# Performance work log

Hardware: AMD Instinct MI355X
Metric: run time of the kernel (lower is better)

## Reference

```python
import jax, jax.numpy as jnp
import numpy as np

B, N, F_IN, T = 8, 1024, 32, 24
E = 16384
K = 3
C_CHEB = 64
C_TIME = 64
TIME_STRIDES = 1
LN_EPS = 1e-5


def setup_inputs() -> dict:
    key = jax.random.key(0)
    ks = jax.random.split(key, 20)
    s = 0.05
    return dict(
        X=jax.random.normal(ks[0], (B, N, F_IN, T), jnp.float32),
        edge_index=jax.random.randint(ks[1], (2, E), 0, N, dtype=jnp.int32),
        # TemporalAttention params
        U1=jax.random.uniform(ks[2], (N,), jnp.float32),
        U2=jax.random.normal(ks[3], (F_IN, N), jnp.float32) * s,
        U3=jax.random.uniform(ks[4], (F_IN,), jnp.float32),
        be=jax.random.normal(ks[5], (1, T, T), jnp.float32) * s,
        Ve=jax.random.normal(ks[6], (T, T), jnp.float32) * s,
        # SpatialAttention params
        W1=jax.random.uniform(ks[7], (T,), jnp.float32),
        W2=jax.random.normal(ks[8], (F_IN, T), jnp.float32) * s,
        W3=jax.random.uniform(ks[9], (F_IN,), jnp.float32),
        bs=jax.random.normal(ks[10], (1, N, N), jnp.float32) * s,
        Vs=jax.random.normal(ks[11], (N, N), jnp.float32) * s,
        # ChebConvAttention params
        cheb_W=jax.random.normal(ks[12], (K, F_IN, C_CHEB), jnp.float32) * s,
        cheb_b=jax.random.uniform(ks[13], (C_CHEB,), jnp.float32),
        # time conv (1x3) and residual conv (1x1), OIHW
        time_W=jax.random.normal(ks[14], (C_TIME, C_CHEB, 1, 3), jnp.float32) * s,
        time_b=jax.random.uniform(ks[15], (C_TIME,), jnp.float32),
        res_W=jax.random.normal(ks[16], (C_TIME, F_IN, 1, 1), jnp.float32) * s,
        res_b=jax.random.uniform(ks[17], (C_TIME,), jnp.float32),
        # layer norm over nb_time_filter channels
        ln_g=jax.random.uniform(ks[18], (C_TIME,), jnp.float32),
        ln_b=jax.random.uniform(ks[19], (C_TIME,), jnp.float32),
    )


def _astgcn_block(X, edge_index, U1, U2, U3, be, Ve, W1, W2, W3, bs, Vs,
                  cheb_W, cheb_b, time_W, time_b, res_W, res_b, ln_g, ln_b):
    Bn, Nn, Fn, Tn = X.shape
    # ---- temporal attention: E_att [B,T,T] ----
    lhs = jnp.einsum('bnft,n->btf', X, U1) @ U2               # [B,T,N]
    rhs = jnp.einsum('f,bnft->bnt', U3, X)                    # [B,N,T]
    Escore = jnp.einsum('ij,bjk->bik', Ve,
                        jax.nn.sigmoid(jnp.einsum('btn,bnu->btu', lhs, rhs) + be))
    E_att = jax.nn.softmax(Escore, axis=1)
    Xt = (X.reshape(Bn, Nn * Fn, Tn) @ E_att).reshape(Bn, Nn, Fn, Tn)
    # ---- spatial attention: S [B,N,N] ----
    slhs = jnp.einsum('bnft,t->bnf', Xt, W1) @ W2             # [B,N,T]
    srhs = jnp.einsum('f,bnft->btn', W3, Xt)                  # [B,T,N]
    Sscore = jnp.einsum('ij,bjk->bik', Vs, jax.nn.sigmoid(slhs @ srhs + bs))
    S = jax.nn.softmax(Sscore, axis=1)
    # ---- scaled Laplacian edge norm (sym normalization, lambda_max = 2) ----
    row, col = edge_index[0], edge_index[1]
    w = (row != col).astype(X.dtype)                          # remove self loops
    deg = jax.ops.segment_sum(w, row, num_segments=Nn)
    dis = jnp.where(deg > 0, jax.lax.rsqrt(jnp.where(deg > 0, deg, 1.0)), 0.0)
    norm = -dis[row] * w * dis[col]                           # [E]; the +1/-1 self loops cancel
    att_norm = norm[None, :] * S[:, row, col]                 # [B,E]

    def prop(x, coef):
        # out[b, r] += coef[(b,)e] * x[b, c] for each edge e=(r,c); x: [B,N,F,T]
        c = coef[None, :, None, None] if coef.ndim == 1 else coef[:, :, None, None]
        msg = c * x[:, col]                                   # [B,E,F,T]
        return jnp.zeros_like(x).at[:, row].add(msg)

    diagS = jnp.diagonal(S, axis1=1, axis2=2)                 # [B,N]
    Tx0 = diagS[:, :, None, None] * X                         # [B,N,F,T]
    out = jnp.einsum('bnft,fo->bnot', Tx0, cheb_W[0])
    Tx1 = prop(Tx0, att_norm)
    out = out + jnp.einsum('bnft,fo->bnot', Tx1, cheb_W[1])
    for k in range(2, cheb_W.shape[0]):
        Tx2 = 2.0 * prop(Tx1, norm) - Tx0
        out = out + jnp.einsum('bnft,fo->bnot', Tx2, cheb_W[k])
        Tx0, Tx1 = Tx1, Tx2
    X_hat = jax.nn.relu(out + cheb_b[None, None, :, None])    # [B,N,Ccheb,T]
    # ---- temporal conv + residual conv + layer norm ----
    dn = ('NCHW', 'OIHW', 'NCHW')
    t_out = jax.lax.conv_general_dilated(
        X_hat.transpose(0, 2, 1, 3), time_W,
        window_strides=(1, TIME_STRIDES), padding=((0, 0), (1, 1)),
        dimension_numbers=dn) + time_b[None, :, None, None]   # [B,Ctime,N,T']
    r_out = jax.lax.conv_general_dilated(
        X.transpose(0, 2, 1, 3), res_W,
        window_strides=(1, TIME_STRIDES), padding=((0, 0), (0, 0)),
        dimension_numbers=dn) + res_b[None, :, None, None]    # [B,Ctime,N,T']
    Z = jax.nn.relu(r_out + t_out).transpose(0, 3, 2, 1)      # [B,T',N,Ctime]
    mu = Z.mean(axis=-1, keepdims=True)
    var = Z.var(axis=-1, keepdims=True)
    Z = (Z - mu) * jax.lax.rsqrt(var + LN_EPS) * ln_g + ln_b
    return Z.transpose(0, 2, 3, 1)                            # [B,N,Ctime,T']


def reference(X, edge_index, U1, U2, U3, be, Ve, W1, W2, W3, bs, Vs,
              cheb_W, cheb_b, time_W, time_b, res_W, res_b, ln_g, ln_b):
    return _astgcn_block(X, edge_index, U1, U2, U3, be, Ve, W1, W2, W3, bs, Vs,
                         cheb_W, cheb_b, time_W, time_b, res_W, res_b, ln_g, ln_b)
```

## Files before the change

### kernel.cpp

```cpp
#include <hip/hip_runtime.h>
#include <hip/hip_bf16.h>
#include <math.h>

#define B_ 8
#define N_ 1024
#define F_ 32
#define T_ 24
#define E_ 16384
#define CC_ 64
#define CT_ 64
#define LN_EPS_ 1e-5f

typedef __attribute__((ext_vector_type(8))) short bf16x8;
typedef __attribute__((ext_vector_type(4))) float f32x4;

__device__ __forceinline__ short f2bf(float f) {
    union { float f; unsigned u; } v; v.f = f;
    unsigned r = v.u + 0x7fffu + ((v.u >> 16) & 1u);
    return (short)(r >> 16);
}


__global__ __launch_bounds__(768) void k_lhs2(const float* __restrict__ X,
                                              const float* __restrict__ U1,
                                              float* __restrict__ out) {
    __shared__ float su[64];
    int b = blockIdx.x >> 4;
    int n0 = (blockIdx.x & 15) * 64;
    int tid = threadIdx.x;
    if (tid < 64) su[tid] = U1[n0 + tid];
    __syncthreads();
    float acc = 0.f;
    const float* xp = X + ((size_t)b * N_ + n0) * 768 + tid;
#pragma unroll 8
    for (int i = 0; i < 64; ++i) acc += xp[(size_t)i * 768] * su[i];
    int f = tid / 24, t = tid - (tid / 24) * 24;
    atomicAdd(&out[b * 768 + t * 32 + f], acc);
}

__global__ void k_lhsN(const float* __restrict__ lhs_tf, const float* __restrict__ U2,
                       float* __restrict__ out) {
    int idx = blockIdx.x * 256 + threadIdx.x;
    if (idx >= B_ * T_ * N_) return;
    int n = idx % N_;
    int bt = idx / N_;
    float acc = 0.f;
#pragma unroll
    for (int f = 0; f < F_; ++f) acc += lhs_tf[bt * F_ + f] * U2[(size_t)f * N_ + n];
    out[idx] = acc;
}

__global__ void k_rhsT(const float* __restrict__ X, const float* __restrict__ U3,
                       float* __restrict__ out) {
    int idx = blockIdx.x * 256 + threadIdx.x;
    if (idx >= B_ * N_ * T_) return;
    int t = idx % T_;
    int n = (idx / T_) % N_;
    int b = idx / (N_ * T_);
    const float* xp = X + ((size_t)(b * N_ + n) * F_) * T_ + t;
    float acc = 0.f;
#pragma unroll
    for (int f = 0; f < F_; ++f) acc += U3[f] * xp[f * T_];
    out[idx] = acc;
}

__global__ __launch_bounds__(256) void k_transp(const float* __restrict__ in,
                                                float* __restrict__ outp) {
    __shared__ float s[64 * 25];
    int b = blockIdx.x >> 4;
    int n0 = (blockIdx.x & 15) * 64;
    int tid = threadIdx.x;
    const float* ip = in + ((size_t)b * N_ + n0) * 24;
    for (int q = tid; q < 1536; q += 256) s[(q / 24) * 25 + (q % 24)] = ip[q];
    __syncthreads();
    for (int q = tid; q < 1536; q += 256) {
        int t = q >> 6, n = q & 63;
        outp[((size_t)b * 24 + t) * N_ + n0 + n] = s[n * 25 + t];
    }
}

__global__ __launch_bounds__(64) void k_edot(const float* __restrict__ lhsN,
                                             const float* __restrict__ rhsTT,
                                             const float* __restrict__ be,
                                             float* __restrict__ sig) {
    int blk = blockIdx.x;
    int b = blk / 576, ij = blk % 576;
    int i = ij / 24, j = ij % 24;
    int lane = threadIdx.x;
    const float* lp = lhsN + ((size_t)b * 24 + i) * N_;
    const float* rp = rhsTT + ((size_t)b * 24 + j) * N_;
    float acc = 0.f;
#pragma unroll
    for (int n = lane; n < N_; n += 64) acc += lp[n] * rp[n];
    for (int off = 32; off > 0; off >>= 1) acc += __shfl_xor(acc, off);
    if (lane == 0) sig[blk] = 1.f / (1.f + expf(-(acc + be[ij])));
}

__global__ __launch_bounds__(576) void k_eatt2(const float* __restrict__ sig,
                                               const float* __restrict__ Ve,
                                               float* __restrict__ Eatt) {
    __shared__ float ss[T_ * T_];
    __shared__ float esc[T_ * T_];
    int b = blockIdx.x;
    int tid = threadIdx.x;
    ss[tid] = sig[b * 576 + tid];
    __syncthreads();
    int i = tid / T_, j = tid % T_;
    {
        float acc = 0.f;
#pragma unroll
        for (int m = 0; m < T_; ++m) acc += Ve[i * T_ + m] * ss[m * T_ + j];
        esc[tid] = acc;
    }
    __syncthreads();
    if (tid < T_) {
        int jj = tid;
        float mx = -1e30f;
        for (int r = 0; r < T_; ++r) mx = fmaxf(mx, esc[r * T_ + jj]);
        float s = 0.f;
        for (int r = 0; r < T_; ++r) {
            float e = expf(esc[r * T_ + jj] - mx);
            ss[r * T_ + jj] = e;
            s += e;
        }
        float inv = 1.f / s;
        for (int r = 0; r < T_; ++r) Eatt[(size_t)(b * T_ + r) * T_ + jj] = ss[r * T_ + jj] * inv;
    }
}

__global__ void k_xt(const float* __restrict__ X, const float* __restrict__ Eatt,
                     float* __restrict__ Xt) {
    __shared__ float e[T_ * T_];
    const int per_b = N_ * F_ * T_ / 256;
    int b = blockIdx.x / per_b;
    int tid = threadIdx.x;
    for (int q = tid; q < T_ * T_; q += 256) e[q] = Eatt[(size_t)b * T_ * T_ + q];
    __syncthreads();
    int off = (blockIdx.x % per_b) * 256 + tid;
    int t = off % T_;
    int nf = off / T_;
    const float* xr = X + ((size_t)b * N_ * F_ + nf) * T_;
    float acc = 0.f;
#pragma unroll
    for (int k = 0; k < T_; ++k) acc += xr[k] * e[k * T_ + t];
    Xt[((size_t)b * N_ * F_ + nf) * T_ + t] = acc;
}


__global__ void k_slhsF(const float* __restrict__ Xt, const float* __restrict__ W1,
                        float* __restrict__ out) {
    int idx = blockIdx.x * 256 + threadIdx.x;
    if (idx >= B_ * N_ * F_) return;
    const float* xp = Xt + (size_t)idx * T_;
    float acc = 0.f;
#pragma unroll
    for (int t = 0; t < T_; ++t) acc += xp[t] * W1[t];
    out[idx] = acc;
}

__global__ void k_slhs(const float* __restrict__ slhsF, const float* __restrict__ W2,
                       float* __restrict__ out) {
    int idx = blockIdx.x * 256 + threadIdx.x;
    if (idx >= B_ * N_ * T_) return;
    int t = idx % T_;
    int bn = idx / T_;
    float acc = 0.f;
#pragma unroll
    for (int f = 0; f < F_; ++f) acc += slhsF[(size_t)bn * F_ + f] * W2[f * T_ + t];
    out[idx] = acc;
}

__global__ void k_srhs(const float* __restrict__ Xt, const float* __restrict__ W3,
                       float* __restrict__ out) {
    int idx = blockIdx.x * 256 + threadIdx.x;
    if (idx >= B_ * N_ * T_) return;
    int t = idx % T_;
    int n = (idx / T_) % N_;
    int b = idx / (N_ * T_);
    const float* xp = Xt + ((size_t)(b * N_ + n) * F_) * T_ + t;
    float acc = 0.f;
#pragma unroll
    for (int f = 0; f < F_; ++f) acc += W3[f] * xp[f * T_];
    out[((size_t)b * T_ + t) * N_ + n] = acc;
}

__global__ __launch_bounds__(256) void k_psig2(const float* __restrict__ slhs,
                                               const float* __restrict__ srhs,
                                               const float* __restrict__ bs,
                                               float* __restrict__ Psig,
                                               __hip_bfloat16* __restrict__ PsigT) {
    __shared__ float sl[64][24];
    __shared__ float sr[24][64];
    __shared__ short st[64][72];
    int b = blockIdx.z;
    int i0 = blockIdx.y * 64, k0 = blockIdx.x * 64;
    int tid = threadIdx.x;
    {
        const float* sp = slhs + ((size_t)b * N_ + i0) * 24;
#pragma unroll
        for (int it = 0; it < 6; ++it) {
            int q = tid + it * 256;
            sl[q / 24][q % 24] = sp[q];
        }
        const float* rp = srhs + (size_t)b * 24 * N_ + k0;
#pragma unroll
        for (int it = 0; it < 6; ++it) {
            int q = tid + it * 256;
            sr[q >> 6][q & 63] = rp[(size_t)(q >> 6) * N_ + (q & 63)];
        }
    }
    __syncthreads();
    int ib = (tid >> 4) * 4;
    int kb = (tid & 15) * 4;
    float acc[4][4];
#pragma unroll
    for (int a = 0; a < 4; ++a) {
        const float4 bv = *(const float4*)(bs + (size_t)(i0 + ib + a) * N_ + k0 + kb);
        acc[a][0] = bv.x; acc[a][1] = bv.y; acc[a][2] = bv.z; acc[a][3] = bv.w;
    }
#pragma unroll
    for (int t = 0; t < 24; ++t) {
        float r0 = sr[t][kb], r1 = sr[t][kb + 1], r2 = sr[t][kb + 2], r3 = sr[t][kb + 3];
#pragma unroll
        for (int a = 0; a < 4; ++a) {
            float lv = sl[ib + a][t];
            acc[a][0] += lv * r0; acc[a][1] += lv * r1; acc[a][2] += lv * r2; acc[a][3] += lv * r3;
        }
    }
#pragma unroll
    for (int a = 0; a < 4; ++a) {
        float4 o;
        o.x = 1.f / (1.f + expf(-acc[a][0]));
        o.y = 1.f / (1.f + expf(-acc[a][1]));
        o.z = 1.f / (1.f + expf(-acc[a][2]));
        o.w = 1.f / (1.f + expf(-acc[a][3]));
        *(float4*)(Psig + (size_t)((size_t)b * N_ + i0 + ib + a) * N_ + k0 + kb) = o;
        st[kb + 0][ib + a] = f2bf(o.x);
        st[kb + 1][ib + a] = f2bf(o.y);
        st[kb + 2][ib + a] = f2bf(o.z);
        st[kb + 3][ib + a] = f2bf(o.w);
    }
    __syncthreads();
    short* op = (short*)PsigT + ((size_t)b * N_ + k0) * N_ + i0;
#pragma unroll
    for (int it = 0; it < 2; ++it) {
        int ch = tid + it * 256;
        int kk = ch >> 3, off = (ch & 7) * 8;
        uint4 u = *(uint4*)&st[kk][off];
        *(uint4*)(op + (size_t)kk * N_ + off) = u;
    }
}

__global__ __launch_bounds__(256) void k_smfma(const float* __restrict__ Vs,
                                               const __hip_bfloat16* __restrict__ PsigT,
                                               float* __restrict__ S) {
    __shared__ short Asd[128][40];
    __shared__ short Bsd[128][40];
    const int b = blockIdx.z;
    const int bm = blockIdx.y * 128, bn = blockIdx.x * 128;
    const int tid = threadIdx.x;
    const int lane = tid & 63, wave = tid >> 6;
    const int wr = wave >> 1, wc = wave & 1;
    const int fr = lane & 15, ks = lane >> 4;
    f32x4 acc[4][4] = {};
    const short* PT = (const short*)PsigT + (size_t)b * N_ * N_;
    for (int k0 = 0; k0 < N_; k0 += 32) {
#pragma unroll
        for (int it = 0; it < 4; ++it) {
            int q = tid + it * 256;
            int row = q >> 3, kk = (q & 7) * 4;
            float4 v = *(const float4*)(Vs + (size_t)(bm + row) * N_ + k0 + kk);
            short4 s4;
            s4.x = f2bf(v.x); s4.y = f2bf(v.y); s4.z = f2bf(v.z); s4.w = f2bf(v.w);
            *(short4*)&Asd[row][kk] = s4;
        }
#pragma unroll
        for (int it = 0; it < 2; ++it) {
            int q = tid + it * 256;
            int row = q >> 2, kk = (q & 3) * 8;
            uint4 u = *(const uint4*)(PT + (size_t)(bn + row) * N_ + k0 + kk);
            *(uint4*)&Bsd[row][kk] = u;
        }
        __syncthreads();
        bf16x8 a[4], bf[4];
#pragma unroll
        for (int m = 0; m < 4; ++m) a[m] = *(const bf16x8*)&Asd[wr * 64 + m * 16 + fr][ks * 8];
#pragma unroll
        for (int n = 0; n < 4; ++n) bf[n] = *(const bf16x8*)&Bsd[wc * 64 + n * 16 + fr][ks * 8];
#pragma unroll
        for (int m = 0; m < 4; ++m)
#pragma unroll
            for (int n = 0; n < 4; ++n)
                acc[m][n] = __builtin_amdgcn_mfma_f32_16x16x32_bf16(a[m], bf[n], acc[m][n], 0, 0, 0);
        __syncthreads();
    }
    float* Sb = S + (size_t)b * N_ * N_;
#pragma unroll
    for (int m = 0; m < 4; ++m)
#pragma unroll
        for (int n = 0; n < 4; ++n) {
#pragma unroll
            for (int j = 0; j < 4; ++j) {
                int row = bm + wr * 64 + m * 16 + (lane >> 4) * 4 + j;
                int col = bn + wc * 64 + n * 16 + (lane & 15);
                Sb[(size_t)row * N_ + col] = acc[m][n][j];
            }
        }
}

__global__ __launch_bounds__(256) void k_smpart(const float* __restrict__ S,
                                                float* __restrict__ pmax,
                                                float* __restrict__ psum) {
    __shared__ float tile[128][64];
    __shared__ float redm[4][64];
    __shared__ float reds[4][64];
    int b = blockIdx.z;
    int chunk = blockIdx.y;
    int cg = blockIdx.x;
    int tid = threadIdx.x;
    const float* Sb = S + (size_t)b * N_ * N_ + (size_t)(chunk * 128) * N_ + cg * 64;
    for (int q = tid; q < 8192; q += 256) {
        int r = q >> 6, c = q & 63;
        tile[r][c] = Sb[(size_t)r * N_ + c];
    }
    __syncthreads();
    int c = tid & 63, grp = tid >> 6;
    float m = -1e30f;
    for (int r = grp; r < 128; r += 4) m = fmaxf(m, tile[r][c]);
    redm[grp][c] = m;
    __syncthreads();
    m = fmaxf(fmaxf(redm[0][c], redm[1][c]), fmaxf(redm[2][c], redm[3][c]));
    float s = 0.f;
    for (int r = grp; r < 128; r += 4) s += __expf(tile[r][c] - m);
    reds[grp][c] = s;
    __syncthreads();
    if (grp == 0) {
        s = reds[0][c] + reds[1][c] + reds[2][c] + reds[3][c];
        size_t o = ((size_t)b * 8 + chunk) * N_ + cg * 64 + c;
        pmax[o] = m;
        psum[o] = s;
    }
}

__global__ __launch_bounds__(1024) void k_smcomb(const float* __restrict__ pmax,
                                                 const float* __restrict__ psum,
                                                 float* __restrict__ colMax,
                                                 float* __restrict__ colInv) {
    int b = blockIdx.x;
    int col = threadIdx.x;
    float M = -1e30f;
#pragma unroll
    for (int ch = 0; ch < 8; ++ch) M = fmaxf(M, pmax[((size_t)b * 8 + ch) * N_ + col]);
    float s = 0.f;
#pragma unroll
    for (int ch = 0; ch < 8; ++ch)
        s += psum[((size_t)b * 8 + ch) * N_ + col] *
             __expf(pmax[((size_t)b * 8 + ch) * N_ + col] - M);
    colMax[(size_t)b * N_ + col] = M;
    colInv[(size_t)b * N_ + col] = 1.f / s;
}


__global__ void k_count(const int* __restrict__ rowI, const int* __restrict__ colI,
                        int* __restrict__ cnt, float* __restrict__ deg) {
    int e = blockIdx.x * 256 + threadIdx.x;
    if (e >= E_) return;
    int r = rowI[e];
    atomicAdd(&cnt[r], 1);
    if (r != colI[e]) atomicAdd(&deg[r], 1.0f);
}

__global__ __launch_bounds__(1024) void k_scan(const int* __restrict__ cnt,
                                               const float* __restrict__ deg,
                                               int* __restrict__ rowPtr,
                                               int* __restrict__ fillPos,
                                               float* __restrict__ dis) {
    __shared__ int s[N_];
    int tid = threadIdx.x;
    int my = cnt[tid];
    s[tid] = my;
    __syncthreads();
    for (int off = 1; off < N_; off <<= 1) {
        int v = 0;
        if (tid >= off) v = s[tid - off];
        __syncthreads();
        s[tid] += v;
        __syncthreads();
    }
    rowPtr[tid + 1] = s[tid];
    if (tid == 0) rowPtr[0] = 0;
    fillPos[tid] = s[tid] - my;
    float d = deg[tid];
    dis[tid] = d > 0.f ? rsqrtf(d) : 0.f;
}

__global__ void k_fill(const int* __restrict__ rowI, const int* __restrict__ colI,
                       int* __restrict__ fillPos, int* __restrict__ csrRow,
                       int* __restrict__ csrCol) {
    int e = blockIdx.x * 256 + threadIdx.x;
    if (e >= E_) return;
    int r = rowI[e];
    int pos = atomicAdd(&fillPos[r], 1);
    csrRow[pos] = r;
    csrCol[pos] = colI[e];
}

__global__ void k_csrcoef(const int* __restrict__ csrRow, const int* __restrict__ csrCol,
                          const float* __restrict__ dis, const float* __restrict__ S,
                          const float* __restrict__ colMax, const float* __restrict__ colInv,
                          float* __restrict__ csrNorm, float* __restrict__ csrAttn) {
    int p = blockIdx.x * 256 + threadIdx.x;
    if (p >= E_) return;
    int r = csrRow[p], c = csrCol[p];
    float nm = (r == c) ? 0.f : -dis[r] * dis[c];
    csrNorm[p] = nm;
    size_t off = (size_t)r * N_ + c;
#pragma unroll
    for (int b = 0; b < B_; ++b) {
        float sv = __expf(S[(size_t)b * N_ * N_ + off] - colMax[(size_t)b * N_ + c]) *
                   colInv[(size_t)b * N_ + c];
        csrAttn[(size_t)b * E_ + p] = nm * sv;
    }
}

__global__ void k_diag(const float* __restrict__ S, const float* __restrict__ colMax,
                       const float* __restrict__ colInv, float* __restrict__ diagS) {
    int idx = blockIdx.x * 256 + threadIdx.x;
    if (idx >= B_ * N_) return;
    int n = idx % N_;
    int b = idx / N_;
    float sv = __expf(S[(size_t)b * N_ * N_ + (size_t)n * N_ + n] - colMax[(size_t)b * N_ + n]) *
               colInv[(size_t)b * N_ + n];
    diagS[idx] = sv;
}

__global__ void k_tx0(const float* __restrict__ X, const float* __restrict__ diagS,
                      float* __restrict__ Tx0) {
    int idx = blockIdx.x * 256 + threadIdx.x;
    if (idx >= B_ * N_ * F_ * T_) return;
    int bn = idx / (F_ * T_);
    Tx0[idx] = diagS[bn] * X[idx];
}

__global__ __launch_bounds__(192) void k_gprop(const float* __restrict__ Tin,
                                               const float* __restrict__ Tsub,
                                               float* __restrict__ Tout,
                                               const float* __restrict__ coef,
                                               const int* __restrict__ csrCol,
                                               const int* __restrict__ rowPtr,
                                               int perB, float scale, int hasSub) {
    int blk = blockIdx.x;
    int b = blk & 7;
    int n = blk >> 3;
    int tid = threadIdx.x;
    int s = rowPtr[n], e = rowPtr[n + 1];
    const float* cbase = coef + (perB ? (size_t)b * E_ : 0);
    float ax = 0.f, ay = 0.f, az = 0.f, aw = 0.f;
    for (int p = s; p < e; ++p) {
        float cf = cbase[p];
        const float4 v =
            *(const float4*)(Tin + ((size_t)(b * N_ + csrCol[p]) * (F_ * T_)) + tid * 4);
        ax += cf * v.x;
        ay += cf * v.y;
        az += cf * v.z;
        aw += cf * v.w;
    }
    size_t obase = (size_t)(b * N_ + n) * (F_ * T_) + tid * 4;
    float4 r;
    r.x = ax * scale;
    r.y = ay * scale;
    r.z = az * scale;
    r.w = aw * scale;
    if (hasSub) {
        const float4 u = *(const float4*)(Tsub + obase);
        r.x -= u.x;
        r.y -= u.y;
        r.z -= u.z;
        r.w -= u.w;
    }
    *(float4*)(Tout + obase) = r;
}

__global__ void k_wprep(const float* __restrict__ tw, const float* __restrict__ rw,
                        float* __restrict__ twT) {
    int idx = blockIdx.x * 256 + threadIdx.x;
    if (idx >= 224 * 64) return;
    int kk = idx >> 6, co = idx & 63;
    twT[idx] = (kk < 192) ? tw[co * 192 + kk] : rw[co * 32 + (kk - 192)];
}

__global__ __launch_bounds__(256) void k_tail(const float* __restrict__ Tx0,
                                              const float* __restrict__ Tx1,
                                              const float* __restrict__ Tx2,
                                              const float* __restrict__ X,
                                              const float* __restrict__ chW,
                                              const float* __restrict__ chb,
                                              const float* __restrict__ twT,
                                              const float* __restrict__ tb,
                                              const float* __restrict__ rb,
                                              const float* __restrict__ lng,
                                              const float* __restrict__ lnb,
                                              float* __restrict__ out) {
    __shared__ float As[32 * 97];
    __shared__ float Bs[32 * 64];
    __shared__ float pool[6656];
    const int tid = threadIdx.x;
    const int site0 = blockIdx.x * 4;
    const int tm = (tid >> 4) * 6;
    const int tn = (tid & 15) * 4;

    for (int q = tid; q < 6656; q += 256) pool[q] = 0.f;

    float chb_r[4], tbrb[4], gam[4], bet[4];
#pragma unroll
    for (int j = 0; j < 4; ++j) {
        chb_r[j] = chb[tn + j];
        tbrb[j] = tb[tn + j] + rb[tn + j];
        gam[j] = lng[tn + j];
        bet[j] = lnb[tn + j];
    }

    float acc[6][4];
#pragma unroll
    for (int i = 0; i < 6; ++i)
#pragma unroll
        for (int j = 0; j < 4; ++j) acc[i][j] = 0.f;

#pragma unroll
    for (int kc = 0; kc < 3; ++kc) {
        const float* Tsel = (kc == 0) ? Tx0 : (kc == 1) ? Tx1 : Tx2;
        const float* gsrc = Tsel + (size_t)site0 * 768;
        __syncthreads();
#pragma unroll
        for (int it = 0; it < 12; ++it) {
            int q = tid + it * 256;
            int ls = q / 768, r = q - ls * 768;
            int k = r / 24, t = r - k * 24;
            As[k * 97 + ls * 24 + t] = gsrc[q];
        }
#pragma unroll
        for (int it = 0; it < 8; ++it) {
            int q = tid + it * 256;
            Bs[q] = chW[kc * 2048 + q];
        }
        __syncthreads();
#pragma unroll
        for (int k = 0; k < 32; ++k) {
            const float4 bv = *(const float4*)&Bs[k * 64 + tn];
#pragma unroll
            for (int i = 0; i < 6; ++i) {
                float a = As[k * 97 + tm + i];
                acc[i][0] += a * bv.x; acc[i][1] += a * bv.y;
                acc[i][2] += a * bv.z; acc[i][3] += a * bv.w;
            }
        }
    }
    __syncthreads();
#pragma unroll
    for (int i = 0; i < 6; ++i) {
        int r = tm + i;
        int ls = r / 24, t = r - ls * 24;
#pragma unroll
        for (int j = 0; j < 4; ++j) {
            pool[ls * 1664 + (tn + j) * 26 + 1 + t] = fmaxf(acc[i][j] + chb_r[j], 0.f);
            acc[i][j] = tbrb[j];
        }
    }

#pragma unroll
    for (int kc = 0; kc < 7; ++kc) {
        const int k0 = kc * 32;
        __syncthreads();
        if (kc < 6) {
#pragma unroll
            for (int it = 0; it < 12; ++it) {
                int q = tid + it * 256;
                int k = q / 96, m = q - k * 96;
                int ls = m / 24, t = m - ls * 24;
                int kk = k0 + k;
                int ci = kk / 3, dt = kk - ci * 3;
                As[k * 97 + m] = pool[ls * 1664 + ci * 26 + t + dt];
            }
        } else {
            const float* gsrc = X + (size_t)site0 * 768;
#pragma unroll
            for (int it = 0; it < 12; ++it) {
                int q = tid + it * 256;
                int ls = q / 768, r = q - ls * 768;
                int k = r / 24, t = r - k * 24;
                As[k * 97 + ls * 24 + t] = gsrc[q];
            }
        }
#pragma unroll
        for (int it = 0; it < 8; ++it) {
            int q = tid + it * 256;
            Bs[q] = twT[k0 * 64 + q];
        }
        __syncthreads();
#pragma unroll
        for (int k = 0; k < 32; ++k) {
            const float4 bv = *(const float4*)&Bs[k * 64 + tn];
#pragma unroll
            for (int i = 0; i < 6; ++i) {
                float a = As[k * 97 + tm + i];
                acc[i][0] += a * bv.x; acc[i][1] += a * bv.y;
                acc[i][2] += a * bv.z; acc[i][3] += a * bv.w;
            }
        }
    }

#pragma unroll
    for (int i = 0; i < 6; ++i) {
        float z0 = fmaxf(acc[i][0], 0.f), z1 = fmaxf(acc[i][1], 0.f);
        float z2 = fmaxf(acc[i][2], 0.f), z3 = fmaxf(acc[i][3], 0.f);
        float s1 = z0 + z1 + z2 + z3;
        float s2 = z0 * z0 + z1 * z1 + z2 * z2 + z3 * z3;
#pragma unroll
        for (int off = 1; off < 16; off <<= 1) {
            s1 += __shfl_xor(s1, off);
            s2 += __shfl_xor(s2, off);
        }
        float mu = s1 * (1.f / 64.f);
        float var = s2 * (1.f / 64.f) - mu * mu;
        float rs = rsqrtf(var + LN_EPS_);
        acc[i][0] = (z0 - mu) * rs * gam[0] + bet[0];
        acc[i][1] = (z1 - mu) * rs * gam[1] + bet[1];
        acc[i][2] = (z2 - mu) * rs * gam[2] + bet[2];
        acc[i][3] = (z3 - mu) * rs * gam[3] + bet[3];
    }
#pragma unroll
    for (int i = 0; i < 6; ++i)
#pragma unroll
        for (int j = 0; j < 4; ++j) pool[(tm + i) * 67 + tn + j] = acc[i][j];
    __syncthreads();
    float* ob = out + (size_t)site0 * 1536;
    for (int q = tid; q < 6144; q += 256) {
        int ls = q / 1536, rem = q - ls * 1536;
        int co = rem / 24, t = rem - co * 24;
        ob[q] = pool[(ls * 24 + t) * 67 + co];
    }
}

extern "C" void kernel_launch(void* const* d_in, const int* in_sizes, int n_in,
                              void* d_out, int out_size, void* d_ws, size_t ws_size,
                              hipStream_t stream) {
    const float* X = (const float*)d_in[0];
    const int* ei = (const int*)d_in[1];
    const float* U1 = (const float*)d_in[2];
    const float* U2 = (const float*)d_in[3];
    const float* U3 = (const float*)d_in[4];
    const float* be = (const float*)d_in[5];
    const float* Ve = (const float*)d_in[6];
    const float* W1 = (const float*)d_in[7];
    const float* W2 = (const float*)d_in[8];
    const float* W3 = (const float*)d_in[9];
    const float* bs = (const float*)d_in[10];
    const float* Vs = (const float*)d_in[11];
    const float* chW = (const float*)d_in[12];
    const float* chb = (const float*)d_in[13];
    const float* tw = (const float*)d_in[14];
    const float* tb = (const float*)d_in[15];
    const float* rw = (const float*)d_in[16];
    const float* rb = (const float*)d_in[17];
    const float* lng = (const float*)d_in[18];
    const float* lnb = (const float*)d_in[19];
    float* out = (float*)d_out;
    float* ws = (float*)d_ws;

    size_t o = 0;
    float* lhs_tf = ws + o; o += B_ * T_ * F_;
    float* lhsN  = ws + o; o += (size_t)B_ * T_ * N_;
    float* rhsT  = ws + o; o += (size_t)B_ * N_ * T_;
    float* rhsTT = ws + o; o += (size_t)B_ * T_ * N_;
    float* sigE  = ws + o; o += B_ * T_ * T_;
    float* Eatt  = ws + o; o += B_ * T_ * T_;
    float* slhsF = ws + o; o += (size_t)B_ * N_ * F_;
    float* slhs  = ws + o; o += (size_t)B_ * N_ * T_;
    float* srhs  = ws + o; o += (size_t)B_ * T_ * N_;
    float* deg   = ws + o; o += N_;
    float* dis   = ws + o; o += N_;
    float* diagS = ws + o; o += B_ * N_;
    float* csrNorm = ws + o; o += E_;
    float* csrAttn = ws + o; o += (size_t)B_ * E_;
    float* pmax  = ws + o; o += (size_t)B_ * 8 * N_;
    float* psum  = ws + o; o += (size_t)B_ * 8 * N_;
    float* colMax = ws + o; o += (size_t)B_ * N_;
    float* colInv = ws + o; o += (size_t)B_ * N_;
    float* twT   = ws + o; o += 224 * 64;
    int* cnt     = (int*)(ws + o); o += N_;
    int* rowPtr  = (int*)(ws + o); o += N_ + 1;
    int* fillPos = (int*)(ws + o); o += N_;
    int* csrRow  = (int*)(ws + o); o += E_;
    int* csrCol  = (int*)(ws + o); o += E_ + 3;
    float* Xt    = ws + o; o += (size_t)B_ * N_ * F_ * T_;
    float* Psig  = ws + o; o += (size_t)B_ * N_ * N_;
    float* S     = ws + o; o += (size_t)B_ * N_ * N_;
    float* Xhat  = ws + o; o += (size_t)B_ * N_ * CC_ * T_;
    float* Tx0 = Psig;
    float* Tx1 = S;
    float* Tx2 = Xt;
    __hip_bfloat16* PsigT = (__hip_bfloat16*)Xhat;
    const int* rowI = ei;
    const int* colI = ei + E_;

    hipMemsetAsync(cnt, 0, N_ * sizeof(int), stream);
    hipMemsetAsync(deg, 0, N_ * sizeof(float), stream);
    k_count<<<(E_ + 255) / 256, 256, 0, stream>>>(rowI, colI, cnt, deg);
    k_scan<<<1, 1024, 0, stream>>>(cnt, deg, rowPtr, fillPos, dis);
    k_fill<<<(E_ + 255) / 256, 256, 0, stream>>>(rowI, colI, fillPos, csrRow, csrCol);
    k_wprep<<<(224 * 64 + 255) / 256, 256, 0, stream>>>(tw, rw, twT);

    hipMemsetAsync(lhs_tf, 0, B_ * T_ * F_ * sizeof(float), stream);
    k_lhs2<<<B_ * 16, 768, 0, stream>>>(X, U1, lhs_tf);
    k_lhsN<<<(B_ * T_ * N_ + 255) / 256, 256, 0, stream>>>(lhs_tf, U2, lhsN);
    k_rhsT<<<(B_ * N_ * T_ + 255) / 256, 256, 0, stream>>>(X, U3, rhsT);
    k_transp<<<B_ * 16, 256, 0, stream>>>(rhsT, rhsTT);
    k_edot<<<B_ * T_ * T_, 64, 0, stream>>>(lhsN, rhsTT, be, sigE);
    k_eatt2<<<B_, 576, 0, stream>>>(sigE, Ve, Eatt);
    k_xt<<<B_ * (N_ * F_ * T_ / 256), 256, 0, stream>>>(X, Eatt, Xt);
    k_slhsF<<<(B_ * N_ * F_ + 255) / 256, 256, 0, stream>>>(Xt, W1, slhsF);
    k_slhs<<<(B_ * N_ * T_ + 255) / 256, 256, 0, stream>>>(slhsF, W2, slhs);
    k_srhs<<<(B_ * N_ * T_ + 255) / 256, 256, 0, stream>>>(Xt, W3, srhs);
    {
        dim3 g(16, 16, B_);
        k_psig2<<<g, 256, 0, stream>>>(slhs, srhs, bs, Psig, PsigT);
    }
    {
        dim3 g(8, 8, B_);
        k_smfma<<<g, 256, 0, stream>>>(Vs, PsigT, S);
    }
    {
        dim3 g(16, 8, B_);
        k_smpart<<<g, 256, 0, stream>>>(S, pmax, psum);
    }
    k_smcomb<<<B_, 1024, 0, stream>>>(pmax, psum, colMax, colInv);
    k_csrcoef<<<(E_ + 255) / 256, 256, 0, stream>>>(csrRow, csrCol, dis, S, colMax, colInv,
                                                    csrNorm, csrAttn);
    k_diag<<<(B_ * N_ + 255) / 256, 256, 0, stream>>>(S, colMax, colInv, diagS);
    k_tx0<<<(B_ * N_ * F_ * T_ + 255) / 256, 256, 0, stream>>>(X, diagS, Tx0);
    k_gprop<<<B_ * N_, 192, 0, stream>>>(Tx0, nullptr, Tx1, csrAttn, csrCol, rowPtr, 1, 1.0f, 0);
    k_gprop<<<B_ * N_, 192, 0, stream>>>(Tx1, Tx0, Tx2, csrNorm, csrCol, rowPtr, 0, 2.0f, 1);
    k_tail<<<B_ * N_ / 4, 256, 0, stream>>>(Tx0, Tx1, Tx2, X, chW, chb, twT, tb, rb,
                                            lng, lnb, out);
}
```

Before: 507.1 us.

## Fuse spatial-attention prep, graph CSR build, and drop unused Psig store

Merges the temporal-attention application (Xt), slhsF, slhs and srhs kernels into one block-tiled kernel, so the large Xt intermediate is never written or reread. It also fuses rhsT with its transpose, combines count/scan/fill/weight-prep into a single-block graph kernel using shared-memory atomics, and removes the fp32 Psig store, which had no remaining reader. Together these cut launches and global traffic. The single-block graph kernel serializes CSR construction onto one CU, and the 24-element register arrays in k_spat may raise register pressure.

```diff
diff --git a/kernel.cpp b/kernel.cpp
--- a/kernel.cpp
+++ b/kernel.cpp
@@ -50,28 +50,24 @@
     out[idx] = acc;
 }
 
-__global__ void k_rhsT(const float* __restrict__ X, const float* __restrict__ U3,
-                       float* __restrict__ out) {
-    int idx = blockIdx.x * 256 + threadIdx.x;
-    if (idx >= B_ * N_ * T_) return;
-    int t = idx % T_;
-    int n = (idx / T_) % N_;
-    int b = idx / (N_ * T_);
-    const float* xp = X + ((size_t)(b * N_ + n) * F_) * T_ + t;
-    float acc = 0.f;
-#pragma unroll
-    for (int f = 0; f < F_; ++f) acc += U3[f] * xp[f * T_];
-    out[idx] = acc;
-}
-
-__global__ __launch_bounds__(256) void k_transp(const float* __restrict__ in,
-                                                float* __restrict__ outp) {
+__global__ __launch_bounds__(256) void k_rhsTT(const float* __restrict__ X,
+                                               const float* __restrict__ U3,
+                                               float* __restrict__ outp) {
     __shared__ float s[64 * 25];
+    __shared__ float su3[32];
     int b = blockIdx.x >> 4;
     int n0 = (blockIdx.x & 15) * 64;
     int tid = threadIdx.x;
-    const float* ip = in + ((size_t)b * N_ + n0) * 24;
-    for (int q = tid; q < 1536; q += 256) s[(q / 24) * 25 + (q % 24)] = ip[q];
+    if (tid < 32) su3[tid] = U3[tid];
+    __syncthreads();
+    for (int q = tid; q < 1536; q += 256) {
+        int n = q / 24, t = q - (q / 24) * 24;
+        const float* xp = X + ((size_t)(b * N_ + n0 + n) * 32) * 24 + t;
+        float acc = 0.f;
+#pragma unroll
+        for (int f = 0; f < 32; ++f) acc += su3[f] * xp[f * 24];
+        s[n * 25 + t] = acc;
+    }
     __syncthreads();
     for (int q = tid; q < 1536; q += 256) {
         int t = q >> 6, n = q & 63;
@@ -128,66 +124,69 @@
     }
 }
 
-__global__ void k_xt(const float* __restrict__ X, const float* __restrict__ Eatt,
-                     float* __restrict__ Xt) {
-    __shared__ float e[T_ * T_];
-    const int per_b = N_ * F_ * T_ / 256;
-    int b = blockIdx.x / per_b;
+__global__ __launch_bounds__(256) void k_spat(const float* __restrict__ X,
+                                              const float* __restrict__ Eatt,
+                                              const float* __restrict__ W1,
+                                              const float* __restrict__ W2,
+                                              const float* __restrict__ W3,
+                                              float* __restrict__ slhs,
+                                              float* __restrict__ srhs) {
+    __shared__ float se[576];
+    __shared__ float sw2[768];
+    __shared__ float sw1[24];
+    __shared__ float sw3[32];
+    __shared__ float scratch[256 * 25];
+    __shared__ float sF[256];
+    int b = blockIdx.x >> 7;
+    int n0 = (blockIdx.x & 127) * 8;
     int tid = threadIdx.x;
-    for (int q = tid; q < T_ * T_; q += 256) e[q] = Eatt[(size_t)b * T_ * T_ + q];
-    __syncthreads();
-    int off = (blockIdx.x % per_b) * 256 + tid;
-    int t = off % T_;
-    int nf = off / T_;
-    const float* xr = X + ((size_t)b * N_ * F_ + nf) * T_;
-    float acc = 0.f;
-#pragma unroll
-    for (int k = 0; k < T_; ++k) acc += xr[k] * e[k * T_ + t];
-    Xt[((size_t)b * N_ * F_ + nf) * T_ + t] = acc;
-}
-
-
-__global__ void k_slhsF(const float* __restrict__ Xt, const float* __restrict__ W1,
-                        float* __restrict__ out) {
-    int idx = blockIdx.x * 256 + threadIdx.x;
-    if (idx >= B_ * N_ * F_) return;
-    const float* xp = Xt + (size_t)idx * T_;
-    float acc = 0.f;
-#pragma unroll
-    for (int t = 0; t < T_; ++t) acc += xp[t] * W1[t];
-    out[idx] = acc;
-}
-
-__global__ void k_slhs(const float* __restrict__ slhsF, const float* __restrict__ W2,
-                       float* __restrict__ out) {
-    int idx = blockIdx.x * 256 + threadIdx.x;
-    if (idx >= B_ * N_ * T_) return;
-    int t = idx % T_;
-    int bn = idx / T_;
-    float acc = 0.f;
-#pragma unroll
-    for (int f = 0; f < F_; ++f) acc += slhsF[(size_t)bn * F_ + f] * W2[f * T_ + t];
-    out[idx] = acc;
-}
-
-__global__ void k_srhs(const float* __restrict__ Xt, const float* __restrict__ W3,
-                       float* __restrict__ out) {
-    int idx = blockIdx.x * 256 + threadIdx.x;
-    if (idx >= B_ * N_ * T_) return;
-    int t = idx % T_;
-    int n = (idx / T_) % N_;
-    int b = idx / (N_ * T_);
-    const float* xp = Xt + ((size_t)(b * N_ + n) * F_) * T_ + t;
-    float acc = 0.f;
-#pragma unroll
-    for (int f = 0; f < F_; ++f) acc += W3[f] * xp[f * T_];
-    out[((size_t)b * T_ + t) * N_ + n] = acc;
+    int n_loc = tid >> 5, f = tid & 31;
+    for (int q = tid; q < 576; q += 256) se[q] = Eatt[b * 576 + q];
+    for (int q = tid; q < 768; q += 256) sw2[q] = W2[q];
+    if (tid < 24) sw1[tid] = W1[tid];
+    if (tid < 32) sw3[tid] = W3[tid];
+    __syncthreads();
+    const float* xp = X + ((size_t)(b * N_ + n0 + n_loc) * 32 + f) * 24;
+    float xr[24];
+#pragma unroll
+    for (int j = 0; j < 6; ++j) {
+        float4 v = *(const float4*)(xp + j * 4);
+        xr[j * 4 + 0] = v.x; xr[j * 4 + 1] = v.y; xr[j * 4 + 2] = v.z; xr[j * 4 + 3] = v.w;
+    }
+    float xt[24];
+#pragma unroll
+    for (int t = 0; t < 24; ++t) xt[t] = 0.f;
+#pragma unroll
+    for (int k = 0; k < 24; ++k) {
+        float xv = xr[k];
+#pragma unroll
+        for (int t = 0; t < 24; ++t) xt[t] += xv * se[k * 24 + t];
+    }
+    float sf = 0.f;
+#pragma unroll
+    for (int t = 0; t < 24; ++t) sf += xt[t] * sw1[t];
+    sF[tid] = sf;
+    float w3v = sw3[f];
+#pragma unroll
+    for (int t = 0; t < 24; ++t) scratch[tid * 25 + t] = w3v * xt[t];
+    __syncthreads();
+    if (tid < 192) {
+        int nl = tid / 24, t = tid - (tid / 24) * 24;
+        float sr_acc = 0.f, sl_acc = 0.f;
+#pragma unroll
+        for (int ff = 0; ff < 32; ++ff) {
+            sr_acc += scratch[(nl * 32 + ff) * 25 + t];
+            sl_acc += sF[nl * 32 + ff] * sw2[ff * 24 + t];
+        }
+        int n = n0 + nl;
+        slhs[((size_t)b * N_ + n) * 24 + t] = sl_acc;
+        srhs[((size_t)b * 24 + t) * N_ + n] = sr_acc;
+    }
 }
 
 __global__ __launch_bounds__(256) void k_psig2(const float* __restrict__ slhs,
                                                const float* __restrict__ srhs,
                                                const float* __restrict__ bs,
-                                               float* __restrict__ Psig,
                                                __hip_bfloat16* __restrict__ PsigT) {
     __shared__ float sl[64][24];
     __shared__ float sr[24][64];
@@ -229,16 +228,10 @@
     }
 #pragma unroll
     for (int a = 0; a < 4; ++a) {
-        float4 o;
-        o.x = 1.f / (1.f + expf(-acc[a][0]));
-        o.y = 1.f / (1.f + expf(-acc[a][1]));
-        o.z = 1.f / (1.f + expf(-acc[a][2]));
-        o.w = 1.f / (1.f + expf(-acc[a][3]));
-        *(float4*)(Psig + (size_t)((size_t)b * N_ + i0 + ib + a) * N_ + k0 + kb) = o;
-        st[kb + 0][ib + a] = f2bf(o.x);
-        st[kb + 1][ib + a] = f2bf(o.y);
-        st[kb + 2][ib + a] = f2bf(o.z);
-        st[kb + 3][ib + a] = f2bf(o.w);
+        st[kb + 0][ib + a] = f2bf(1.f / (1.f + expf(-acc[a][0])));
+        st[kb + 1][ib + a] = f2bf(1.f / (1.f + expf(-acc[a][1])));
+        st[kb + 2][ib + a] = f2bf(1.f / (1.f + expf(-acc[a][2])));
+        st[kb + 3][ib + a] = f2bf(1.f / (1.f + expf(-acc[a][3])));
     }
     __syncthreads();
     short* op = (short*)PsigT + ((size_t)b * N_ + k0) * N_ + i0;
@@ -360,25 +353,31 @@
     colInv[(size_t)b * N_ + col] = 1.f / s;
 }
 
-
-__global__ void k_count(const int* __restrict__ rowI, const int* __restrict__ colI,
-                        int* __restrict__ cnt, float* __restrict__ deg) {
-    int e = blockIdx.x * 256 + threadIdx.x;
-    if (e >= E_) return;
-    int r = rowI[e];
-    atomicAdd(&cnt[r], 1);
-    if (r != colI[e]) atomicAdd(&deg[r], 1.0f);
-}
-
-__global__ __launch_bounds__(1024) void k_scan(const int* __restrict__ cnt,
-                                               const float* __restrict__ deg,
-                                               int* __restrict__ rowPtr,
-                                               int* __restrict__ fillPos,
-                                               float* __restrict__ dis) {
+__global__ __launch_bounds__(1024) void k_graph(const int* __restrict__ rowI,
+                                                const int* __restrict__ colI,
+                                                const float* __restrict__ tw,
+                                                const float* __restrict__ rw,
+                                                int* __restrict__ rowPtr,
+                                                int* __restrict__ csrRow,
+                                                int* __restrict__ csrCol,
+                                                float* __restrict__ dis,
+                                                float* __restrict__ twT) {
     __shared__ int s[N_];
+    __shared__ int fillPos[N_];
+    __shared__ int degc[N_];
     int tid = threadIdx.x;
-    int my = cnt[tid];
-    s[tid] = my;
+    s[tid] = 0;
+    degc[tid] = 0;
+    __syncthreads();
+#pragma unroll
+    for (int i = 0; i < 16; ++i) {
+        int e = tid + i * 1024;
+        int r = rowI[e], c = colI[e];
+        atomicAdd(&s[r], 1);
+        if (r != c) atomicAdd(&degc[r], 1);
+    }
+    __syncthreads();
+    int my = s[tid];
     __syncthreads();
     for (int off = 1; off < N_; off <<= 1) {
         int v = 0;
@@ -390,19 +389,21 @@
     rowPtr[tid + 1] = s[tid];
     if (tid == 0) rowPtr[0] = 0;
     fillPos[tid] = s[tid] - my;
-    float d = deg[tid];
+    float d = (float)degc[tid];
     dis[tid] = d > 0.f ? rsqrtf(d) : 0.f;
-}
-
-__global__ void k_fill(const int* __restrict__ rowI, const int* __restrict__ colI,
-                       int* __restrict__ fillPos, int* __restrict__ csrRow,
-                       int* __restrict__ csrCol) {
-    int e = blockIdx.x * 256 + threadIdx.x;
-    if (e >= E_) return;
-    int r = rowI[e];
-    int pos = atomicAdd(&fillPos[r], 1);
-    csrRow[pos] = r;
-    csrCol[pos] = colI[e];
+    __syncthreads();
+#pragma unroll
+    for (int i = 0; i < 16; ++i) {
+        int e = tid + i * 1024;
+        int r = rowI[e];
+        int pos = atomicAdd(&fillPos[r], 1);
+        csrRow[pos] = r;
+        csrCol[pos] = colI[e];
+    }
+    for (int q = tid; q < 224 * 64; q += 1024) {
+        int kk = q >> 6, co = q & 63;
+        twT[q] = (kk < 192) ? tw[co * 192 + kk] : rw[co * 32 + (kk - 192)];
+    }
 }
 
 __global__ void k_csrcoef(const int* __restrict__ csrRow, const int* __restrict__ csrCol,
@@ -479,14 +480,6 @@
         r.w -= u.w;
     }
     *(float4*)(Tout + obase) = r;
-}
-
-__global__ void k_wprep(const float* __restrict__ tw, const float* __restrict__ rw,
-                        float* __restrict__ twT) {
-    int idx = blockIdx.x * 256 + threadIdx.x;
-    if (idx >= 224 * 64) return;
-    int kk = idx >> 6, co = idx & 63;
-    twT[idx] = (kk < 192) ? tw[co * 192 + kk] : rw[co * 32 + (kk - 192)];
 }
 
 __global__ __launch_bounds__(256) void k_tail(const float* __restrict__ Tx0,
@@ -670,14 +663,11 @@
     size_t o = 0;
     float* lhs_tf = ws + o; o += B_ * T_ * F_;
     float* lhsN  = ws + o; o += (size_t)B_ * T_ * N_;
-    float* rhsT  = ws + o; o += (size_t)B_ * N_ * T_;
     float* rhsTT = ws + o; o += (size_t)B_ * T_ * N_;
     float* sigE  = ws + o; o += B_ * T_ * T_;
     float* Eatt  = ws + o; o += B_ * T_ * T_;
-    float* slhsF = ws + o; o += (size_t)B_ * N_ * F_;
     float* slhs  = ws + o; o += (size_t)B_ * N_ * T_;
     float* srhs  = ws + o; o += (size_t)B_ * T_ * N_;
-    float* deg   = ws + o; o += N_;
     float* dis   = ws + o; o += N_;
     float* diagS = ws + o; o += B_ * N_;
     float* csrNorm = ws + o; o += E_;
@@ -687,9 +677,7 @@
     float* colMax = ws + o; o += (size_t)B_ * N_;
     float* colInv = ws + o; o += (size_t)B_ * N_;
     float* twT   = ws + o; o += 224 * 64;
-    int* cnt     = (int*)(ws + o); o += N_;
     int* rowPtr  = (int*)(ws + o); o += N_ + 1;
-    int* fillPos = (int*)(ws + o); o += N_;
     int* csrRow  = (int*)(ws + o); o += E_;
     int* csrCol  = (int*)(ws + o); o += E_ + 3;
     float* Xt    = ws + o; o += (size_t)B_ * N_ * F_ * T_;
@@ -703,27 +691,18 @@
     const int* rowI = ei;
     const int* colI = ei + E_;
 
-    hipMemsetAsync(cnt, 0, N_ * sizeof(int), stream);
-    hipMemsetAsync(deg, 0, N_ * sizeof(float), stream);
-    k_count<<<(E_ + 255) / 256, 256, 0, stream>>>(rowI, colI, cnt, deg);
-    k_scan<<<1, 1024, 0, stream>>>(cnt, deg, rowPtr, fillPos, dis);
-    k_fill<<<(E_ + 255) / 256, 256, 0, stream>>>(rowI, colI, fillPos, csrRow, csrCol);
-    k_wprep<<<(224 * 64 + 255) / 256, 256, 0, stream>>>(tw, rw, twT);
+    k_graph<<<1, 1024, 0, stream>>>(rowI, colI, tw, rw, rowPtr, csrRow, csrCol, dis, twT);
 
     hipMemsetAsync(lhs_tf, 0, B_ * T_ * F_ * sizeof(float), stream);
     k_lhs2<<<B_ * 16, 768, 0, stream>>>(X, U1, lhs_tf);
     k_lhsN<<<(B_ * T_ * N_ + 255) / 256, 256, 0, stream>>>(lhs_tf, U2, lhsN);
-    k_rhsT<<<(B_ * N_ * T_ + 255) / 256, 256, 0, stream>>>(X, U3, rhsT);
-    k_transp<<<B_ * 16, 256, 0, stream>>>(rhsT, rhsTT);
+    k_rhsTT<<<B_ * 16, 256, 0, stream>>>(X, U3, rhsTT);
     k_edot<<<B_ * T_ * T_, 64, 0, stream>>>(lhsN, rhsTT, be, sigE);
     k_eatt2<<<B_, 576, 0, stream>>>(sigE, Ve, Eatt);
-    k_xt<<<B_ * (N_ * F_ * T_ / 256), 256, 0, stream>>>(X, Eatt, Xt);
-    k_slhsF<<<(B_ * N_ * F_ + 255) / 256, 256, 0, stream>>>(Xt, W1, slhsF);
-    k_slhs<<<(B_ * N_ * T_ + 255) / 256, 256, 0, stream>>>(slhsF, W2, slhs);
-    k_srhs<<<(B_ * N_ * T_ + 255) / 256, 256, 0, stream>>>(Xt, W3, srhs);
+    k_spat<<<B_ * 128, 256, 0, stream>>>(X, Eatt, W1, W2, W3, slhs, srhs);
     {
         dim3 g(16, 16, B_);
-        k_psig2<<<g, 256, 0, stream>>>(slhs, srhs, bs, Psig, PsigT);
+        k_psig2<<<g, 256, 0, stream>>>(slhs, srhs, bs, PsigT);
     }
     {
         dim3 g(8, 8, B_);
```

New measurement: 476.0 us. -6.1%, faster.
